# Optimization experiments

Measured on AMD Instinct MI355X. Metric: run time of the kernel, lower is better.

The kernel has to match this reference:

```python
import jax, jax.numpy as jnp
import numpy as np

N = 100000
E = 1600000
F_IN = 602
NHID = 128
N_CLS = 41


def setup_inputs() -> dict:
    key = jax.random.key(0)
    k1, k2, k3, k4 = jax.random.split(key, 4)
    x = jax.random.normal(k1, (N, F_IN), dtype=jnp.float32)
    edge_index = jax.random.randint(k2, (2, E), 0, N, dtype=jnp.int64)
    # Glorot-style scaled weights
    W1 = jax.random.normal(k3, (F_IN, NHID), dtype=jnp.float32) * (1.0 / np.sqrt(F_IN))
    b1 = jnp.zeros((NHID,), dtype=jnp.float32)
    W2 = jax.random.normal(k4, (NHID, N_CLS), dtype=jnp.float32) * (1.0 / np.sqrt(NHID))
    b2 = jnp.zeros((N_CLS,), dtype=jnp.float32)
    return {"x": x, "edge_index": edge_index, "W1": W1, "b1": b1, "W2": W2, "b2": b2}


def reference(x, edge_index, W1, b1, W2, b2):
    n = x.shape[0]
    loop = jnp.arange(n, dtype=edge_index.dtype)
    # PyG GCNConv: add self-loops, symmetric normalization D^-1/2 (A+I) D^-1/2
    src = jnp.concatenate([edge_index[0], loop])  # [E+N]
    dst = jnp.concatenate([edge_index[1], loop])  # [E+N]
    ones = jnp.ones(src.shape[0], dtype=x.dtype)
    deg = jax.ops.segment_sum(ones, dst, num_segments=n)  # in-degree incl self-loop
    dinv = jnp.where(deg > 0, jax.lax.rsqrt(deg), 0.0)
    norm = dinv[src] * dinv[dst]  # [E+N]

    def conv(h, W, b):
        h = h @ W  # transform first (smaller feature dim for gather)
        msg = h[src] * norm[:, None]  # gather + scale
        return jax.ops.segment_sum(msg, dst, num_segments=n) + b  # scatter-add

    h = jax.nn.relu(conv(x, W1, b1))
    # dropout is identity in eval mode
    out = conv(h, W2, b2)
    return jax.nn.log_softmax(out, axis=1)
```

## Files before the change

kernel.cpp:

```cpp
#include <hip/hip_runtime.h>
#include <math.h>

#define GK 602
#define GH 128
#define GC 41
#define GCP 48
#define KPAD 608
#define NKT 19

typedef __bf16 bf16x8 __attribute__((ext_vector_type(8)));
typedef float f32x16 __attribute__((ext_vector_type(16)));

__device__ __forceinline__ unsigned short f2bf(float f) {
    __bf16 b = (__bf16)f;
    return __builtin_bit_cast(unsigned short, b);
}
__device__ __forceinline__ float bf2f(unsigned short u) {
    return __uint_as_float((unsigned int)u << 16);
}
__device__ __forceinline__ float bflo(unsigned int u) { return __uint_as_float(u << 16); }
__device__ __forceinline__ float bfhi(unsigned int u) { return __uint_as_float(u & 0xffff0000u); }

__device__ __forceinline__ void gl_lds16(const float* g, float* l) {
    __builtin_amdgcn_global_load_lds((const __attribute__((address_space(1))) void*)g,
                                     (__attribute__((address_space(3))) void*)l, 16, 0, 0);
}
__device__ __forceinline__ void gl_lds4(const float* g, float* l) {
    __builtin_amdgcn_global_load_lds((const __attribute__((address_space(1))) void*)g,
                                     (__attribute__((address_space(3))) void*)l, 4, 0, 0);
}


__global__ void k_hist(const int* __restrict__ dst, int* __restrict__ counts, int E) {
    int e = blockIdx.x * 256 + threadIdx.x;
    if (e < E) atomicAdd(&counts[dst[e]], 1);
}

__global__ void k_scan_a(const int* __restrict__ counts, int* __restrict__ row_ptr,
                         int* __restrict__ bsum, int n) {
    __shared__ int wsum[4];
    int t = threadIdx.x;
    int lane = t & 63;
    int wv = t >> 6;
    int base = blockIdx.x * 1024 + t * 4;
    int v[4];
    int s = 0;
#pragma unroll
    for (int j = 0; j < 4; ++j) {
        int idx = base + j;
        v[j] = (idx < n) ? counts[idx] : 0;
        s += v[j];
    }
    int incl = s;
#pragma unroll
    for (int o = 1; o < 64; o <<= 1) {
        int x = __shfl_up(incl, o);
        if (lane >= o) incl += x;
    }
    if (lane == 63) wsum[wv] = incl;
    __syncthreads();
    int woff = 0;
#pragma unroll
    for (int i = 0; i < 3; ++i) woff += (i < wv) ? wsum[i] : 0;
    if (t == 255) bsum[blockIdx.x] = woff + incl;
    int off = woff + incl - s;
#pragma unroll
    for (int j = 0; j < 4; ++j) {
        int idx = base + j;
        if (idx < n) row_ptr[idx] = off;
        off += v[j];
    }
}

__global__ void k_scan_b(int* __restrict__ bsum, int nb) {
    __shared__ int sh[256];
    int t = threadIdx.x;
    int v = (t < nb) ? bsum[t] : 0;
    sh[t] = v;
    __syncthreads();
    for (int o = 1; o < 256; o <<= 1) {
        int x = (t >= o) ? sh[t - o] : 0;
        __syncthreads();
        sh[t] += x;
        __syncthreads();
    }
    if (t < nb) bsum[t] = sh[t] - v;
}

__global__ void k_scan_c(int* __restrict__ row_ptr, const int* __restrict__ bsum,
                         const int* __restrict__ counts, float* __restrict__ dinv,
                         int* __restrict__ cursor, int n, int E) {
    int i = blockIdx.x * 256 + threadIdx.x;
    if (i < n) {
        int rp = row_ptr[i] + bsum[i >> 10];
        row_ptr[i] = rp;
        cursor[i] = rp;
        dinv[i] = rsqrtf((float)(counts[i] + 1));
    }
    if (i == 0) row_ptr[n] = E;
}

__global__ void k_fill(const int* __restrict__ src, const int* __restrict__ dst,
                       const float* __restrict__ dinv,
                       int* __restrict__ cursor, int2* __restrict__ meta, int E) {
    int e = blockIdx.x * 256 + threadIdx.x;
    if (e < E) {
        int s = src[e];
        int d = dst[e];
        int p = atomicAdd(&cursor[d], 1);
        float w = dinv[s] * dinv[d];
        meta[p] = make_int2(s, __float_as_int(w));
    }
}


__global__ void k_prepW1F(const float* __restrict__ W1, unsigned short* __restrict__ W1F) {
    int i = blockIdx.x * 256 + threadIdx.x;
    if (i >= NKT * 4096) return;
    int kt = i >> 12;
    int r  = i & 4095;
    int nt = r >> 10;
    int r2 = r & 1023;
    int bs = r2 >> 9;
    int r3 = r2 & 511;
    int ln = r3 >> 3;
    int j  = r3 & 7;
    int col = 32 * nt + (ln & 31);
    int k   = 32 * kt + 16 * bs + 8 * (ln >> 5) + j;
    float v = (k < GK) ? W1[(size_t)k * GH + col] : 0.f;
    W1F[i] = f2bf(v);
}


#define SLABF (32 * GK)
#define CH16  (SLABF / 4)

__global__ __launch_bounds__(256, 2) void k_gemm1_mfma(const float* __restrict__ X,
                                                       const unsigned short* __restrict__ W1F,
                                                       unsigned short* __restrict__ Y, int M) {
    __shared__ float As[SLABF + 16];
    int tid = threadIdx.x;
    int lane = tid & 63;
    int w = tid >> 6;
    int rowBase = blockIdx.x * 32;
    const float* slab = X + (size_t)rowBase * GK;

#pragma unroll
    for (int r = 0; r < 18; ++r) {
        int c = tid + 256 * r;
        gl_lds16(slab + 4 * c, &As[4 * c]);
    }
    if (w < 3) {
        int c = 4608 + (w << 6) + lane;
        gl_lds16(slab + 4 * c, &As[4 * c]);
    } else {
        int f = 19200 + lane;
        gl_lds4(slab + f, &As[f]);
    }
    if (tid < 16) As[SLABF + tid] = 0.f;
    asm volatile("s_waitcnt vmcnt(0)" ::: "memory");
    __syncthreads();

    int arow = lane & 31;
    int kh = 8 * (lane >> 5);
    const float* Ar = &As[arow * GK];
    const unsigned short* Wb = W1F + (size_t)w * 1024 + (size_t)lane * 8;

    f32x16 acc;
#pragma unroll
    for (int i = 0; i < 16; ++i) acc[i] = 0.f;

#pragma unroll
    for (int t = 0; t < NKT; ++t) {
        const unsigned short* Wt = Wb + (size_t)t * 4096;
        bf16x8 b0 = *(const bf16x8*)(Wt);
        bf16x8 b1 = *(const bf16x8*)(Wt + 512);
        const float* a0p = Ar + 32 * t + kh;
        float2 p0 = *(const float2*)(a0p + 0);
        float2 p1 = *(const float2*)(a0p + 2);
        float2 p2 = *(const float2*)(a0p + 4);
        float2 p3 = *(const float2*)(a0p + 6);
        const float* a1p = a0p + 16;
        float2 q0 = *(const float2*)(a1p + 0);
        float2 q1 = *(const float2*)(a1p + 2);
        float2 q2 = *(const float2*)(a1p + 4);
        float2 q3 = *(const float2*)(a1p + 6);
        bf16x8 af0, af1;
        af0[0] = (__bf16)p0.x; af0[1] = (__bf16)p0.y;
        af0[2] = (__bf16)p1.x; af0[3] = (__bf16)p1.y;
        af0[4] = (__bf16)p2.x; af0[5] = (__bf16)p2.y;
        af0[6] = (__bf16)p3.x; af0[7] = (__bf16)p3.y;
        af1[0] = (__bf16)q0.x; af1[1] = (__bf16)q0.y;
        af1[2] = (__bf16)q1.x; af1[3] = (__bf16)q1.y;
        af1[4] = (__bf16)q2.x; af1[5] = (__bf16)q2.y;
        af1[6] = (__bf16)q3.x; af1[7] = (__bf16)q3.y;
        acc = __builtin_amdgcn_mfma_f32_32x32x16_bf16(af0, b0, acc, 0, 0, 0);
        acc = __builtin_amdgcn_mfma_f32_32x32x16_bf16(af1, b1, acc, 0, 0, 0);
    }

    int gcol = 32 * w + (lane & 31);
#pragma unroll
    for (int reg = 0; reg < 16; ++reg) {
        int rrow = (reg & 3) + 8 * (reg >> 2) + 4 * (lane >> 5);
        int grow = rowBase + rrow;
        if (grow < M) Y[(size_t)grow * GH + gcol] = f2bf(acc[reg]);
    }
}


__global__ __launch_bounds__(256) void k_agg1(const unsigned int* __restrict__ H,
                                              unsigned int* __restrict__ O,
                                              const int* __restrict__ row_ptr,
                                              const int2* __restrict__ meta,
                                              const float* __restrict__ dinv,
                                              const float* __restrict__ bias, int n) {
    int wv = threadIdx.x >> 6;
    int lane = threadIdx.x & 63;
    int d = blockIdx.x * 4 + wv;
    if (d >= n) return;
    float dd = dinv[d];
    int beg = row_ptr[d], end = row_ptr[d + 1];
    unsigned int v = H[(size_t)d * 64 + lane];
    float sw = dd * dd;
    float a0 = sw * bflo(v);
    float a1 = sw * bfhi(v);
    int e = beg;
    for (; e + 16 <= end; e += 16) {
        int2 m[16];
        unsigned int u[16];
#pragma unroll
        for (int j = 0; j < 16; ++j) m[j] = meta[e + j];
#pragma unroll
        for (int j = 0; j < 16; ++j) u[j] = H[(size_t)m[j].x * 64 + lane];
#pragma unroll
        for (int j = 0; j < 16; ++j) {
            float wj = __int_as_float(m[j].y);
            a0 = fmaf(wj, bflo(u[j]), a0);
            a1 = fmaf(wj, bfhi(u[j]), a1);
        }
    }
    if (e + 8 <= end) {
        int2 m[8];
        unsigned int u[8];
#pragma unroll
        for (int j = 0; j < 8; ++j) m[j] = meta[e + j];
#pragma unroll
        for (int j = 0; j < 8; ++j) u[j] = H[(size_t)m[j].x * 64 + lane];
#pragma unroll
        for (int j = 0; j < 8; ++j) {
            float wj = __int_as_float(m[j].y);
            a0 = fmaf(wj, bflo(u[j]), a0);
            a1 = fmaf(wj, bfhi(u[j]), a1);
        }
        e += 8;
    }
    if (e + 4 <= end) {
        int2 m[4];
        unsigned int u[4];
#pragma unroll
        for (int j = 0; j < 4; ++j) m[j] = meta[e + j];
#pragma unroll
        for (int j = 0; j < 4; ++j) u[j] = H[(size_t)m[j].x * 64 + lane];
#pragma unroll
        for (int j = 0; j < 4; ++j) {
            float wj = __int_as_float(m[j].y);
            a0 = fmaf(wj, bflo(u[j]), a0);
            a1 = fmaf(wj, bfhi(u[j]), a1);
        }
        e += 4;
    }
    for (; e < end; ++e) {
        int2 m = meta[e];
        unsigned int u = H[(size_t)m.x * 64 + lane];
        float wj = __int_as_float(m.y);
        a0 = fmaf(wj, bflo(u), a0);
        a1 = fmaf(wj, bfhi(u), a1);
    }
    a0 = fmaxf(a0 + bias[2 * lane], 0.f);
    a1 = fmaxf(a1 + bias[2 * lane + 1], 0.f);
    O[(size_t)d * 64 + lane] = (unsigned int)f2bf(a0) | ((unsigned int)f2bf(a1) << 16);
}


__global__ __launch_bounds__(256) void k_gemm2t(const unsigned int* __restrict__ Hb,
                                                const float* __restrict__ W2,
                                                unsigned short* __restrict__ G, int n) {
    __shared__ float ws[128][GCP];
    for (int i = threadIdx.x; i < 128 * GCP; i += 256) {
        int k = i / GCP;
        int c = i - k * GCP;
        ws[k][c] = (c < GC) ? W2[k * GC + c] : 0.f;
    }
    __syncthreads();
    int r0 = blockIdx.x * 512 + threadIdx.x;
    int r1 = r0 + 256;
    bool v0 = r0 < n, v1 = r1 < n;
    float acc0[GCP], acc1[GCP];
#pragma unroll
    for (int c = 0; c < GCP; ++c) { acc0[c] = 0.f; acc1[c] = 0.f; }
    const uint2* h0 = (const uint2*)(Hb + (size_t)(v0 ? r0 : 0) * 64);
    const uint2* h1 = (const uint2*)(Hb + (size_t)(v1 ? r1 : 0) * 64);
    for (int q = 0; q < 32; ++q) {
        uint2 ua = h0[q];
        uint2 ub = h1[q];
        float va[4] = {bflo(ua.x), bfhi(ua.x), bflo(ua.y), bfhi(ua.y)};
        float vb[4] = {bflo(ub.x), bfhi(ub.x), bflo(ub.y), bfhi(ub.y)};
#pragma unroll
        for (int j = 0; j < 4; ++j) {
            int k = 4 * q + j;
#pragma unroll
            for (int cq = 0; cq < GCP / 4; ++cq) {
                float4 wv = *(const float4*)&ws[k][4 * cq];
                acc0[4 * cq + 0] = fmaf(va[j], wv.x, acc0[4 * cq + 0]);
                acc0[4 * cq + 1] = fmaf(va[j], wv.y, acc0[4 * cq + 1]);
                acc0[4 * cq + 2] = fmaf(va[j], wv.z, acc0[4 * cq + 2]);
                acc0[4 * cq + 3] = fmaf(va[j], wv.w, acc0[4 * cq + 3]);
                acc1[4 * cq + 0] = fmaf(vb[j], wv.x, acc1[4 * cq + 0]);
                acc1[4 * cq + 1] = fmaf(vb[j], wv.y, acc1[4 * cq + 1]);
                acc1[4 * cq + 2] = fmaf(vb[j], wv.z, acc1[4 * cq + 2]);
                acc1[4 * cq + 3] = fmaf(vb[j], wv.w, acc1[4 * cq + 3]);
            }
        }
    }
    if (v0) {
#pragma unroll
        for (int c = 0; c < GCP; ++c) G[(size_t)r0 * GCP + c] = f2bf(acc0[c]);
    }
    if (v1) {
#pragma unroll
        for (int c = 0; c < GCP; ++c) G[(size_t)r1 * GCP + c] = f2bf(acc1[c]);
    }
}


__global__ __launch_bounds__(256) void k_agg2(const unsigned short* __restrict__ G,
                                              float* __restrict__ out,
                                              const int* __restrict__ row_ptr,
                                              const int2* __restrict__ meta,
                                              const float* __restrict__ dinv,
                                              const float* __restrict__ b2, int n) {
    int wv = threadIdx.x >> 6;
    int lane = threadIdx.x & 63;
    int gl = (lane < GCP) ? lane : (GCP - 1);
    int d = blockIdx.x * 4 + wv;
    if (d >= n) return;
    float dd = dinv[d];
    int beg = row_ptr[d], end = row_ptr[d + 1];
    float a = dd * dd * bf2f(G[(size_t)d * GCP + gl]);
    int e = beg;
    for (; e + 16 <= end; e += 16) {
        int2 m[16];
        unsigned short u[16];
#pragma unroll
        for (int j = 0; j < 16; ++j) m[j] = meta[e + j];
#pragma unroll
        for (int j = 0; j < 16; ++j) u[j] = G[(size_t)m[j].x * GCP + gl];
#pragma unroll
        for (int j = 0; j < 16; ++j) a = fmaf(__int_as_float(m[j].y), bf2f(u[j]), a);
    }
    if (e + 8 <= end) {
        int2 m[8];
        unsigned short u[8];
#pragma unroll
        for (int j = 0; j < 8; ++j) m[j] = meta[e + j];
#pragma unroll
        for (int j = 0; j < 8; ++j) u[j] = G[(size_t)m[j].x * GCP + gl];
#pragma unroll
        for (int j = 0; j < 8; ++j) a = fmaf(__int_as_float(m[j].y), bf2f(u[j]), a);
        e += 8;
    }
    if (e + 4 <= end) {
        int2 m[4];
        unsigned short u[4];
#pragma unroll
        for (int j = 0; j < 4; ++j) m[j] = meta[e + j];
#pragma unroll
        for (int j = 0; j < 4; ++j) u[j] = G[(size_t)m[j].x * GCP + gl];
#pragma unroll
        for (int j = 0; j < 4; ++j) a = fmaf(__int_as_float(m[j].y), bf2f(u[j]), a);
        e += 4;
    }
    for (; e < end; ++e) {
        int2 m = meta[e];
        a = fmaf(__int_as_float(m.y), bf2f(G[(size_t)m.x * GCP + gl]), a);
    }
    float logit = (lane < GC) ? (a + b2[lane]) : -INFINITY;
    float mx = logit;
#pragma unroll
    for (int off = 32; off; off >>= 1) mx = fmaxf(mx, __shfl_xor(mx, off));
    float ex = (lane < GC) ? __expf(logit - mx) : 0.f;
    float sm = ex;
#pragma unroll
    for (int off = 32; off; off >>= 1) sm += __shfl_xor(sm, off);
    if (lane < GC) out[(size_t)d * GC + lane] = logit - mx - __logf(sm);
}


static inline size_t alignup256(size_t x) { return (x + 255) & ~(size_t)255; }

extern "C" void kernel_launch(void* const* d_in, const int* in_sizes, int n_in,
                              void* d_out, int out_size, void* d_ws, size_t ws_size,
                              hipStream_t stream) {
    const float* x  = (const float*)d_in[0];
    const int*   ei = (const int*)d_in[1];
    const float* W1 = (const float*)d_in[2];
    const float* b1 = (const float*)d_in[3];
    const float* W2 = (const float*)d_in[4];
    const float* b2 = (const float*)d_in[5];
    float* out = (float*)d_out;

    const int n = in_sizes[0] / GK;
    const int E = in_sizes[1] / 2;
    const int* src = ei;
    const int* dst = ei + E;

    char* w = (char*)d_ws;
    char* p;
    p = w; w += alignup256((size_t)n * 4);            float* dinv  = (float*)p;
    p = w; w += alignup256((size_t)n * 4);            int* counts  = (int*)p;
    p = w; w += alignup256((size_t)n * 4);            int* cursor  = (int*)p;
    p = w; w += alignup256((size_t)(n + 1) * 4);      int* row_ptr = (int*)p;
    p = w; w += alignup256(1024 * 4);                 int* bsum    = (int*)p;
    p = w; w += alignup256((size_t)E * 8);            int2* meta   = (int2*)p;
    p = w; w += alignup256((size_t)GH * KPAD * 2);    unsigned short* W1F = (unsigned short*)p;
    p = w; w += alignup256((size_t)n * GH * 2);       unsigned short* bufA = (unsigned short*)p;
    p = w; w += alignup256((size_t)n * GH * 2);       unsigned short* bufB = (unsigned short*)p;
    p = w; w += alignup256((size_t)n * GCP * 2);      unsigned short* G    = (unsigned short*)p;

    hipMemsetAsync(counts, 0, (size_t)n * 4, stream);

    int gE = (E + 255) / 256;
    int gN = (n + 255) / 256;
    int nb = (n + 1023) / 1024;

    k_hist<<<gE, 256, 0, stream>>>(dst, counts, E);
    k_scan_a<<<nb, 256, 0, stream>>>(counts, row_ptr, bsum, n);
    k_scan_b<<<1, 256, 0, stream>>>(bsum, nb);
    k_scan_c<<<gN, 256, 0, stream>>>(row_ptr, bsum, counts, dinv, cursor, n, E);
    k_fill<<<gE, 256, 0, stream>>>(src, dst, dinv, cursor, meta, E);

    k_prepW1F<<<(NKT * 4096 + 255) / 256, 256, 0, stream>>>(W1, W1F);
    k_gemm1_mfma<<<(n + 31) / 32, 256, 0, stream>>>(x, W1F, bufA, n);
    k_agg1<<<(n + 3) / 4, 256, 0, stream>>>((const unsigned int*)bufA, (unsigned int*)bufB,
                                            row_ptr, meta, dinv, b1, n);
    k_gemm2t<<<(n + 511) / 512, 256, 0, stream>>>((const unsigned int*)bufB, W2, G, n);
    k_agg2<<<(n + 3) / 4, 256, 0, stream>>>(G, out, row_ptr, meta, dinv, b2, n);
}
```

Baseline: 679.9 us.

## Fuse second-layer GEMM into layer-1 aggregation and vectorize edge preprocessing

The relu'd layer-1 aggregate for each node is staged in LDS, and a 128x48 matvec against a pre-transposed W2 runs inside the aggregation kernel. This removes the separate gemm2 kernel and the round trip of the hidden bf16 buffer through global memory. The histogram and CSR fill kernels now process four edges per thread using int4 loads. W2 transposition is folded into the weight-prep kernel. The trade-off is extra per-wave work in the aggregation tail, with only 48 of 64 lanes active, and W2T being re-read from global/L2 by every wave.

```diff
diff --git a/kernel.cpp b/kernel.cpp
--- a/kernel.cpp
+++ b/kernel.cpp
@@ -7,6 +7,8 @@
 #define GCP 48
 #define KPAD 608
 #define NKT 19
+#define W1FN (NKT * 4096)
+#define W2TN (GCP * 128)
 
 typedef __bf16 bf16x8 __attribute__((ext_vector_type(8)));
 typedef float f32x16 __attribute__((ext_vector_type(16)));
@@ -32,8 +34,21 @@
 
 
 __global__ void k_hist(const int* __restrict__ dst, int* __restrict__ counts, int E) {
-    int e = blockIdx.x * 256 + threadIdx.x;
-    if (e < E) atomicAdd(&counts[dst[e]], 1);
+    int g = blockIdx.x * 256 + threadIdx.x;
+    int base = g * 4;
+    if (((E & 3) == 0) && (base + 3 < E)) {
+        int4 d4 = *(const int4*)(dst + base);
+        atomicAdd(&counts[d4.x], 1);
+        atomicAdd(&counts[d4.y], 1);
+        atomicAdd(&counts[d4.z], 1);
+        atomicAdd(&counts[d4.w], 1);
+    } else {
+#pragma unroll
+        for (int j = 0; j < 4; ++j) {
+            int e = base + j;
+            if (e < E) atomicAdd(&counts[dst[e]], 1);
+        }
+    }
 }
 
 __global__ void k_scan_a(const int* __restrict__ counts, int* __restrict__ row_ptr,
@@ -103,37 +118,61 @@
 __global__ void k_fill(const int* __restrict__ src, const int* __restrict__ dst,
                        const float* __restrict__ dinv,
                        int* __restrict__ cursor, int2* __restrict__ meta, int E) {
-    int e = blockIdx.x * 256 + threadIdx.x;
-    if (e < E) {
-        int s = src[e];
-        int d = dst[e];
-        int p = atomicAdd(&cursor[d], 1);
-        float w = dinv[s] * dinv[d];
-        meta[p] = make_int2(s, __float_as_int(w));
-    }
-}
-
-
-__global__ void k_prepW1F(const float* __restrict__ W1, unsigned short* __restrict__ W1F) {
+    int g = blockIdx.x * 256 + threadIdx.x;
+    int base = g * 4;
+    if (((E & 3) == 0) && (base + 3 < E)) {
+        int4 s4 = *(const int4*)(src + base);
+        int4 d4 = *(const int4*)(dst + base);
+        int ss[4] = {s4.x, s4.y, s4.z, s4.w};
+        int dd[4] = {d4.x, d4.y, d4.z, d4.w};
+#pragma unroll
+        for (int j = 0; j < 4; ++j) {
+            int p = atomicAdd(&cursor[dd[j]], 1);
+            float w = dinv[ss[j]] * dinv[dd[j]];
+            meta[p] = make_int2(ss[j], __float_as_int(w));
+        }
+    } else {
+#pragma unroll
+        for (int j = 0; j < 4; ++j) {
+            int e = base + j;
+            if (e < E) {
+                int s = src[e];
+                int d = dst[e];
+                int p = atomicAdd(&cursor[d], 1);
+                float w = dinv[s] * dinv[d];
+                meta[p] = make_int2(s, __float_as_int(w));
+            }
+        }
+    }
+}
+
+
+__global__ void k_prepW(const float* __restrict__ W1, unsigned short* __restrict__ W1F,
+                        const float* __restrict__ W2, float* __restrict__ W2T) {
     int i = blockIdx.x * 256 + threadIdx.x;
-    if (i >= NKT * 4096) return;
-    int kt = i >> 12;
-    int r  = i & 4095;
-    int nt = r >> 10;
-    int r2 = r & 1023;
-    int bs = r2 >> 9;
-    int r3 = r2 & 511;
-    int ln = r3 >> 3;
-    int j  = r3 & 7;
-    int col = 32 * nt + (ln & 31);
-    int k   = 32 * kt + 16 * bs + 8 * (ln >> 5) + j;
-    float v = (k < GK) ? W1[(size_t)k * GH + col] : 0.f;
-    W1F[i] = f2bf(v);
+    if (i < W1FN) {
+        int kt = i >> 12;
+        int r  = i & 4095;
+        int nt = r >> 10;
+        int r2 = r & 1023;
+        int bs = r2 >> 9;
+        int r3 = r2 & 511;
+        int ln = r3 >> 3;
+        int j  = r3 & 7;
+        int col = 32 * nt + (ln & 31);
+        int k   = 32 * kt + 16 * bs + 8 * (ln >> 5) + j;
+        float v = (k < GK) ? W1[(size_t)k * GH + col] : 0.f;
+        W1F[i] = f2bf(v);
+    } else if (i < W1FN + W2TN) {
+        int j = i - W1FN;
+        int c = j >> 7;
+        int k = j & 127;
+        W2T[j] = (c < GC) ? W2[k * GC + c] : 0.f;
+    }
 }
 
 
 #define SLABF (32 * GK)
-#define CH16  (SLABF / 4)
 
 __global__ __launch_bounds__(256, 2) void k_gemm1_mfma(const float* __restrict__ X,
                                                        const unsigned short* __restrict__ W1F,
@@ -208,12 +247,14 @@
 }
 
 
-__global__ __launch_bounds__(256) void k_agg1(const unsigned int* __restrict__ H,
-                                              unsigned int* __restrict__ O,
-                                              const int* __restrict__ row_ptr,
-                                              const int2* __restrict__ meta,
-                                              const float* __restrict__ dinv,
-                                              const float* __restrict__ bias, int n) {
+__global__ __launch_bounds__(256) void k_agg1f(const unsigned int* __restrict__ H,
+                                               unsigned short* __restrict__ G,
+                                               const int* __restrict__ row_ptr,
+                                               const int2* __restrict__ meta,
+                                               const float* __restrict__ dinv,
+                                               const float* __restrict__ bias,
+                                               const float* __restrict__ W2T, int n) {
+    __shared__ float hs[4][128];
     int wv = threadIdx.x >> 6;
     int lane = threadIdx.x & 63;
     int d = blockIdx.x * 4 + wv;
@@ -278,57 +319,26 @@
     }
     a0 = fmaxf(a0 + bias[2 * lane], 0.f);
     a1 = fmaxf(a1 + bias[2 * lane + 1], 0.f);
-    O[(size_t)d * 64 + lane] = (unsigned int)f2bf(a0) | ((unsigned int)f2bf(a1) << 16);
-}
-
-
-__global__ __launch_bounds__(256) void k_gemm2t(const unsigned int* __restrict__ Hb,
-                                                const float* __restrict__ W2,
-                                                unsigned short* __restrict__ G, int n) {
-    __shared__ float ws[128][GCP];
-    for (int i = threadIdx.x; i < 128 * GCP; i += 256) {
-        int k = i / GCP;
-        int c = i - k * GCP;
-        ws[k][c] = (c < GC) ? W2[k * GC + c] : 0.f;
-    }
-    __syncthreads();
-    int r0 = blockIdx.x * 512 + threadIdx.x;
-    int r1 = r0 + 256;
-    bool v0 = r0 < n, v1 = r1 < n;
-    float acc0[GCP], acc1[GCP];
-#pragma unroll
-    for (int c = 0; c < GCP; ++c) { acc0[c] = 0.f; acc1[c] = 0.f; }
-    const uint2* h0 = (const uint2*)(Hb + (size_t)(v0 ? r0 : 0) * 64);
-    const uint2* h1 = (const uint2*)(Hb + (size_t)(v1 ? r1 : 0) * 64);
-    for (int q = 0; q < 32; ++q) {
-        uint2 ua = h0[q];
-        uint2 ub = h1[q];
-        float va[4] = {bflo(ua.x), bfhi(ua.x), bflo(ua.y), bfhi(ua.y)};
-        float vb[4] = {bflo(ub.x), bfhi(ub.x), bflo(ub.y), bfhi(ub.y)};
-#pragma unroll
-        for (int j = 0; j < 4; ++j) {
-            int k = 4 * q + j;
-#pragma unroll
-            for (int cq = 0; cq < GCP / 4; ++cq) {
-                float4 wv = *(const float4*)&ws[k][4 * cq];
-                acc0[4 * cq + 0] = fmaf(va[j], wv.x, acc0[4 * cq + 0]);
-                acc0[4 * cq + 1] = fmaf(va[j], wv.y, acc0[4 * cq + 1]);
-                acc0[4 * cq + 2] = fmaf(va[j], wv.z, acc0[4 * cq + 2]);
-                acc0[4 * cq + 3] = fmaf(va[j], wv.w, acc0[4 * cq + 3]);
-                acc1[4 * cq + 0] = fmaf(vb[j], wv.x, acc1[4 * cq + 0]);
-                acc1[4 * cq + 1] = fmaf(vb[j], wv.y, acc1[4 * cq + 1]);
-                acc1[4 * cq + 2] = fmaf(vb[j], wv.z, acc1[4 * cq + 2]);
-                acc1[4 * cq + 3] = fmaf(vb[j], wv.w, acc1[4 * cq + 3]);
-            }
-        }
-    }
-    if (v0) {
-#pragma unroll
-        for (int c = 0; c < GCP; ++c) G[(size_t)r0 * GCP + c] = f2bf(acc0[c]);
-    }
-    if (v1) {
-#pragma unroll
-        for (int c = 0; c < GCP; ++c) G[(size_t)r1 * GCP + c] = f2bf(acc1[c]);
+
+    *(float2*)&hs[wv][2 * lane] = make_float2(a0, a1);
+    asm volatile("s_waitcnt lgkmcnt(0)" ::: "memory");
+    __builtin_amdgcn_sched_barrier(0);
+
+    if (lane < GCP) {
+        const float* wr = W2T + (size_t)lane * 128;
+        float s0 = 0.f, s1 = 0.f;
+#pragma unroll
+        for (int q = 0; q < 16; ++q) {
+            float4 wv0 = *(const float4*)(wr + 8 * q);
+            float4 wv1 = *(const float4*)(wr + 8 * q + 4);
+            float4 h0 = *(const float4*)&hs[wv][8 * q];
+            float4 h1 = *(const float4*)&hs[wv][8 * q + 4];
+            s0 = fmaf(wv0.x, h0.x, s0); s0 = fmaf(wv0.y, h0.y, s0);
+            s0 = fmaf(wv0.z, h0.z, s0); s0 = fmaf(wv0.w, h0.w, s0);
+            s1 = fmaf(wv1.x, h1.x, s1); s1 = fmaf(wv1.y, h1.y, s1);
+            s1 = fmaf(wv1.z, h1.z, s1); s1 = fmaf(wv1.w, h1.w, s1);
+        }
+        G[(size_t)d * GCP + lane] = f2bf(s0 + s1);
     }
 }
 
@@ -423,26 +433,25 @@
     p = w; w += alignup256(1024 * 4);                 int* bsum    = (int*)p;
     p = w; w += alignup256((size_t)E * 8);            int2* meta   = (int2*)p;
     p = w; w += alignup256((size_t)GH * KPAD * 2);    unsigned short* W1F = (unsigned short*)p;
+    p = w; w += alignup256((size_t)W2TN * 4);         float* W2T = (float*)p;
     p = w; w += alignup256((size_t)n * GH * 2);       unsigned short* bufA = (unsigned short*)p;
-    p = w; w += alignup256((size_t)n * GH * 2);       unsigned short* bufB = (unsigned short*)p;
     p = w; w += alignup256((size_t)n * GCP * 2);      unsigned short* G    = (unsigned short*)p;
 
     hipMemsetAsync(counts, 0, (size_t)n * 4, stream);
 
-    int gE = (E + 255) / 256;
+    int gE4 = (E + 1023) / 1024;
     int gN = (n + 255) / 256;
     int nb = (n + 1023) / 1024;
 
-    k_hist<<<gE, 256, 0, stream>>>(dst, counts, E);
+    k_hist<<<gE4, 256, 0, stream>>>(dst, counts, E);
     k_scan_a<<<nb, 256, 0, stream>>>(counts, row_ptr, bsum, n);
     k_scan_b<<<1, 256, 0, stream>>>(bsum, nb);
     k_scan_c<<<gN, 256, 0, stream>>>(row_ptr, bsum, counts, dinv, cursor, n, E);
-    k_fill<<<gE, 256, 0, stream>>>(src, dst, dinv, cursor, meta, E);
-
-    k_prepW1F<<<(NKT * 4096 + 255) / 256, 256, 0, stream>>>(W1, W1F);
+    k_fill<<<gE4, 256, 0, stream>>>(src, dst, dinv, cursor, meta, E);
+
+    k_prepW<<<(W1FN + W2TN + 255) / 256, 256, 0, stream>>>(W1, W1F, W2, W2T);
     k_gemm1_mfma<<<(n + 31) / 32, 256, 0, stream>>>(x, W1F, bufA, n);
-    k_agg1<<<(n + 3) / 4, 256, 0, stream>>>((const unsigned int*)bufA, (unsigned int*)bufB,
-                                            row_ptr, meta, dinv, b1, n);
-    k_gemm2t<<<(n + 511) / 512, 256, 0, stream>>>((const unsigned int*)bufB, W2, G, n);
+    k_agg1f<<<(n + 3) / 4, 256, 0, stream>>>((const unsigned int*)bufA, G,
+                                             row_ptr, meta, dinv, b1, W2T, n);
     k_agg2<<<(n + 3) / 4, 256, 0, stream>>>(G, out, row_ptr, meta, dinv, b2, n);
 }
```

After: 906.8 us. +33.4%, slower.

## Store only source indices in CSR and recompute edge weights from dinv in aggregation

Applied to the files above, without the earlier changes.

The CSR edge array now stores only the source index (4 bytes) instead of an (index, weight) pair (8 bytes). The aggregation kernels gather dinv[src] per edge and apply the destination's dinv once at the end, rather than reading a precomputed per-edge weight. The hist and fill kernels also process four edges per thread with int4 loads, and fill no longer reads dinv. This halves edge-metadata traffic and the fill's scattered writes, at the cost of an extra random 4-byte gather per edge in both aggregation passes.

```diff
diff --git a/kernel.cpp b/kernel.cpp
--- a/kernel.cpp
+++ b/kernel.cpp
@@ -32,8 +32,21 @@
 
 
 __global__ void k_hist(const int* __restrict__ dst, int* __restrict__ counts, int E) {
-    int e = blockIdx.x * 256 + threadIdx.x;
-    if (e < E) atomicAdd(&counts[dst[e]], 1);
+    int g = blockIdx.x * 256 + threadIdx.x;
+    int base = g * 4;
+    if (((E & 3) == 0) && (base + 3 < E)) {
+        int4 d4 = *(const int4*)(dst + base);
+        atomicAdd(&counts[d4.x], 1);
+        atomicAdd(&counts[d4.y], 1);
+        atomicAdd(&counts[d4.z], 1);
+        atomicAdd(&counts[d4.w], 1);
+    } else {
+#pragma unroll
+        for (int j = 0; j < 4; ++j) {
+            int e = base + j;
+            if (e < E) atomicAdd(&counts[dst[e]], 1);
+        }
+    }
 }
 
 __global__ void k_scan_a(const int* __restrict__ counts, int* __restrict__ row_ptr,
@@ -101,15 +114,28 @@
 }
 
 __global__ void k_fill(const int* __restrict__ src, const int* __restrict__ dst,
-                       const float* __restrict__ dinv,
-                       int* __restrict__ cursor, int2* __restrict__ meta, int E) {
-    int e = blockIdx.x * 256 + threadIdx.x;
-    if (e < E) {
-        int s = src[e];
-        int d = dst[e];
-        int p = atomicAdd(&cursor[d], 1);
-        float w = dinv[s] * dinv[d];
-        meta[p] = make_int2(s, __float_as_int(w));
+                       int* __restrict__ cursor, int* __restrict__ meta, int E) {
+    int g = blockIdx.x * 256 + threadIdx.x;
+    int base = g * 4;
+    if (((E & 3) == 0) && (base + 3 < E)) {
+        int4 s4 = *(const int4*)(src + base);
+        int4 d4 = *(const int4*)(dst + base);
+        int ss[4] = {s4.x, s4.y, s4.z, s4.w};
+        int dd[4] = {d4.x, d4.y, d4.z, d4.w};
+#pragma unroll
+        for (int j = 0; j < 4; ++j) {
+            int p = atomicAdd(&cursor[dd[j]], 1);
+            meta[p] = ss[j];
+        }
+    } else {
+#pragma unroll
+        for (int j = 0; j < 4; ++j) {
+            int e = base + j;
+            if (e < E) {
+                int p = atomicAdd(&cursor[dst[e]], 1);
+                meta[p] = src[e];
+            }
+        }
     }
 }
 
@@ -133,7 +159,6 @@
 
 
 #define SLABF (32 * GK)
-#define CH16  (SLABF / 4)
 
 __global__ __launch_bounds__(256, 2) void k_gemm1_mfma(const float* __restrict__ X,
                                                        const unsigned short* __restrict__ W1F,
@@ -211,7 +236,7 @@
 __global__ __launch_bounds__(256) void k_agg1(const unsigned int* __restrict__ H,
                                               unsigned int* __restrict__ O,
                                               const int* __restrict__ row_ptr,
-                                              const int2* __restrict__ meta,
+                                              const int* __restrict__ meta,
                                               const float* __restrict__ dinv,
                                               const float* __restrict__ bias, int n) {
     int wv = threadIdx.x >> 6;
@@ -221,63 +246,68 @@
     float dd = dinv[d];
     int beg = row_ptr[d], end = row_ptr[d + 1];
     unsigned int v = H[(size_t)d * 64 + lane];
-    float sw = dd * dd;
-    float a0 = sw * bflo(v);
-    float a1 = sw * bfhi(v);
+    float a0 = dd * bflo(v);
+    float a1 = dd * bfhi(v);
     int e = beg;
     for (; e + 16 <= end; e += 16) {
-        int2 m[16];
+        int m[16];
         unsigned int u[16];
+        float ws[16];
 #pragma unroll
         for (int j = 0; j < 16; ++j) m[j] = meta[e + j];
 #pragma unroll
-        for (int j = 0; j < 16; ++j) u[j] = H[(size_t)m[j].x * 64 + lane];
+        for (int j = 0; j < 16; ++j) u[j] = H[(size_t)m[j] * 64 + lane];
+#pragma unroll
+        for (int j = 0; j < 16; ++j) ws[j] = dinv[m[j]];
 #pragma unroll
         for (int j = 0; j < 16; ++j) {
-            float wj = __int_as_float(m[j].y);
-            a0 = fmaf(wj, bflo(u[j]), a0);
-            a1 = fmaf(wj, bfhi(u[j]), a1);
+            a0 = fmaf(ws[j], bflo(u[j]), a0);
+            a1 = fmaf(ws[j], bfhi(u[j]), a1);
         }
     }
     if (e + 8 <= end) {
-        int2 m[8];
+        int m[8];
         unsigned int u[8];
+        float ws[8];
 #pragma unroll
         for (int j = 0; j < 8; ++j) m[j] = meta[e + j];
 #pragma unroll
-        for (int j = 0; j < 8; ++j) u[j] = H[(size_t)m[j].x * 64 + lane];
+        for (int j = 0; j < 8; ++j) u[j] = H[(size_t)m[j] * 64 + lane];
+#pragma unroll
+        for (int j = 0; j < 8; ++j) ws[j] = dinv[m[j]];
 #pragma unroll
         for (int j = 0; j < 8; ++j) {
-            float wj = __int_as_float(m[j].y);
-            a0 = fmaf(wj, bflo(u[j]), a0);
-            a1 = fmaf(wj, bfhi(u[j]), a1);
+            a0 = fmaf(ws[j], bflo(u[j]), a0);
+            a1 = fmaf(ws[j], bfhi(u[j]), a1);
         }
         e += 8;
     }
     if (e + 4 <= end) {
-        int2 m[4];
+        int m[4];
         unsigned int u[4];
+        float ws[4];
 #pragma unroll
         for (int j = 0; j < 4; ++j) m[j] = meta[e + j];
 #pragma unroll
-        for (int j = 0; j < 4; ++j) u[j] = H[(size_t)m[j].x * 64 + lane];
+        for (int j = 0; j < 4; ++j) u[j] = H[(size_t)m[j] * 64 + lane];
+#pragma unroll
+        for (int j = 0; j < 4; ++j) ws[j] = dinv[m[j]];
 #pragma unroll
         for (int j = 0; j < 4; ++j) {
-            float wj = __int_as_float(m[j].y);
-            a0 = fmaf(wj, bflo(u[j]), a0);
-            a1 = fmaf(wj, bfhi(u[j]), a1);
+            a0 = fmaf(ws[j], bflo(u[j]), a0);
+            a1 = fmaf(ws[j], bfhi(u[j]), a1);
         }
         e += 4;
     }
     for (; e < end; ++e) {
-        int2 m = meta[e];
-        unsigned int u = H[(size_t)m.x * 64 + lane];
-        float wj = __int_as_float(m.y);
+        int m = meta[e];
+        unsigned int u = H[(size_t)m * 64 + lane];
+        float wj = dinv[m];
         a0 = fmaf(wj, bflo(u), a0);
         a1 = fmaf(wj, bfhi(u), a1);
     }
-    a0 = fmaxf(a0 + bias[2 * lane], 0.f);
-    a1 = fmaxf(a1 + bias[2 * lane + 1], 0.f);
+    a0 = fmaxf(fmaf(dd, a0, bias[2 * lane]), 0.f);
+    a1 = fmaxf(fmaf(dd, a1, bias[2 * lane + 1]), 0.f);
     O[(size_t)d * 64 + lane] = (unsigned int)f2bf(a0) | ((unsigned int)f2bf(a1) << 16);
 }
 
@@ -336,7 +366,7 @@
 __global__ __launch_bounds__(256) void k_agg2(const unsigned short* __restrict__ G,
                                               float* __restrict__ out,
                                               const int* __restrict__ row_ptr,
-                                              const int2* __restrict__ meta,
+                                              const int* __restrict__ meta,
                                               const float* __restrict__ dinv,
                                               const float* __restrict__ b2, int n) {
     int wv = threadIdx.x >> 6;
@@ -346,45 +376,54 @@
     if (d >= n) return;
     float dd = dinv[d];
     int beg = row_ptr[d], end = row_ptr[d + 1];
-    float a = dd * dd * bf2f(G[(size_t)d * GCP + gl]);
+    float a = dd * bf2f(G[(size_t)d * GCP + gl]);
     int e = beg;
     for (; e + 16 <= end; e += 16) {
-        int2 m[16];
+        int m[16];
         unsigned short u[16];
+        float ws[16];
 #pragma unroll
         for (int j = 0; j < 16; ++j) m[j] = meta[e + j];
 #pragma unroll
-        for (int j = 0; j < 16; ++j) u[j] = G[(size_t)m[j].x * GCP + gl];
-#pragma unroll
-        for (int j = 0; j < 16; ++j) a = fmaf(__int_as_float(m[j].y), bf2f(u[j]), a);
+        for (int j = 0; j < 16; ++j) u[j] = G[(size_t)m[j] * GCP + gl];
+#pragma unroll
+        for (int j = 0; j < 16; ++j) ws[j] = dinv[m[j]];
+#pragma unroll
+        for (int j = 0; j < 16; ++j) a = fmaf(ws[j], bf2f(u[j]), a);
     }
     if (e + 8 <= end) {
-        int2 m[8];
+        int m[8];
         unsigned short u[8];
+        float ws[8];
 #pragma unroll
         for (int j = 0; j < 8; ++j) m[j] = meta[e + j];
 #pragma unroll
-        for (int j = 0; j < 8; ++j) u[j] = G[(size_t)m[j].x * GCP + gl];
-#pragma unroll
-        for (int j = 0; j < 8; ++j) a = fmaf(__int_as_float(m[j].y), bf2f(u[j]), a);
+        for (int j = 0; j < 8; ++j) u[j] = G[(size_t)m[j] * GCP + gl];
+#pragma unroll
+        for (int j = 0; j < 8; ++j) ws[j] = dinv[m[j]];
+#pragma unroll
+        for (int j = 0; j < 8; ++j) a = fmaf(ws[j], bf2f(u[j]), a);
         e += 8;
     }
     if (e + 4 <= end) {
-        int2 m[4];
+        int m[4];
         unsigned short u[4];
+        float ws[4];
 #pragma unroll
         for (int j = 0; j < 4; ++j) m[j] = meta[e + j];
 #pragma unroll
-        for (int j = 0; j < 4; ++j) u[j] = G[(size_t)m[j].x * GCP + gl];
-#pragma unroll
-        for (int j = 0; j < 4; ++j) a = fmaf(__int_as_float(m[j].y), bf2f(u[j]), a);
+        for (int j = 0; j < 4; ++j) u[j] = G[(size_t)m[j] * GCP + gl];
+#pragma unroll
+        for (int j = 0; j < 4; ++j) ws[j] = dinv[m[j]];
+#pragma unroll
+        for (int j = 0; j < 4; ++j) a = fmaf(ws[j], bf2f(u[j]), a);
         e += 4;
     }
     for (; e < end; ++e) {
-        int2 m = meta[e];
-        a = fmaf(__int_as_float(m.y), bf2f(G[(size_t)m.x * GCP + gl]), a);
-    }
-    float logit = (lane < GC) ? (a + b2[lane]) : -INFINITY;
+        int m = meta[e];
+        a = fmaf(dinv[m], bf2f(G[(size_t)m * GCP + gl]), a);
+    }
+    float logit = (lane < GC) ? fmaf(dd, a, b2[lane]) : -INFINITY;
     float mx = logit;
 #pragma unroll
     for (int off = 32; off; off >>= 1) mx = fmaxf(mx, __shfl_xor(mx, off));
@@ -421,7 +460,7 @@
     p = w; w += alignup256((size_t)n * 4);            int* cursor  = (int*)p;
     p = w; w += alignup256((size_t)(n + 1) * 4);      int* row_ptr = (int*)p;
     p = w; w += alignup256(1024 * 4);                 int* bsum    = (int*)p;
-    p = w; w += alignup256((size_t)E * 8);            int2* meta   = (int2*)p;
+    p = w; w += alignup256((size_t)E * 4);            int* meta    = (int*)p;
     p = w; w += alignup256((size_t)GH * KPAD * 2);    unsigned short* W1F = (unsigned short*)p;
     p = w; w += alignup256((size_t)n * GH * 2);       unsigned short* bufA = (unsigned short*)p;
     p = w; w += alignup256((size_t)n * GH * 2);       unsigned short* bufB = (unsigned short*)p;
@@ -429,15 +468,15 @@
 
     hipMemsetAsync(counts, 0, (size_t)n * 4, stream);
 
-    int gE = (E + 255) / 256;
+    int gE4 = (E + 1023) / 1024;
     int gN = (n + 255) / 256;
     int nb = (n + 1023) / 1024;
 
-    k_hist<<<gE, 256, 0, stream>>>(dst, counts, E);
+    k_hist<<<gE4, 256, 0, stream>>>(dst, counts, E);
     k_scan_a<<<nb, 256, 0, stream>>>(counts, row_ptr, bsum, n);
     k_scan_b<<<1, 256, 0, stream>>>(bsum, nb);
     k_scan_c<<<gN, 256, 0, stream>>>(row_ptr, bsum, counts, dinv, cursor, n, E);
-    k_fill<<<gE, 256, 0, stream>>>(src, dst, dinv, cursor, meta, E);
+    k_fill<<<gE4, 256, 0, stream>>>(src, dst, cursor, meta, E);
 
     k_prepW1F<<<(NKT * 4096 + 255) / 256, 256, 0, stream>>>(W1, W1F);
     k_gemm1_mfma<<<(n + 31) / 32, 256, 0, stream>>>(x, W1F, bufA, n);
```

Measured after the change: 763.9 us. +12.3%, slower.

## Merge W1 prep with histogram and CSR fill with GEMM1 via block-range dispatch

Applied to the files above, without the earlier changes.

Fuses the W1 bf16 reformat and the degree histogram into one launch, and fuses the CSR fill pass into the GEMM1 launch, using disjoint block ranges so the independent work can run concurrently. Each histogram/fill thread now handles four edges with vectorized int4 loads. This removes two kernel launches and lets the latency-bound atomic scatter overlap with the compute-heavy GEMM. The fill blocks inherit GEMM1's launch bounds and its shared-memory allocation, which may reduce their occupancy.

```diff
diff --git a/kernel.cpp b/kernel.cpp
--- a/kernel.cpp
+++ b/kernel.cpp
@@ -7,6 +7,7 @@
 #define GCP 48
 #define KPAD 608
 #define NKT 19
+#define W1FN (NKT * 4096)
 
 typedef __bf16 bf16x8 __attribute__((ext_vector_type(8)));
 typedef float f32x16 __attribute__((ext_vector_type(16)));
@@ -31,9 +32,41 @@
 }
 
 
-__global__ void k_hist(const int* __restrict__ dst, int* __restrict__ counts, int E) {
-    int e = blockIdx.x * 256 + threadIdx.x;
-    if (e < E) atomicAdd(&counts[dst[e]], 1);
+__global__ void k_pre(const float* __restrict__ W1, unsigned short* __restrict__ W1F,
+                      const int* __restrict__ dst, int* __restrict__ counts,
+                      int E, int nbPrep) {
+    if ((int)blockIdx.x < nbPrep) {
+        int i = blockIdx.x * 256 + threadIdx.x;
+        if (i >= W1FN) return;
+        int kt = i >> 12;
+        int r  = i & 4095;
+        int nt = r >> 10;
+        int r2 = r & 1023;
+        int bs = r2 >> 9;
+        int r3 = r2 & 511;
+        int ln = r3 >> 3;
+        int j  = r3 & 7;
+        int col = 32 * nt + (ln & 31);
+        int k   = 32 * kt + 16 * bs + 8 * (ln >> 5) + j;
+        float v = (k < GK) ? W1[(size_t)k * GH + col] : 0.f;
+        W1F[i] = f2bf(v);
+    } else {
+        int g = (blockIdx.x - nbPrep) * 256 + threadIdx.x;
+        int base = g * 4;
+        if (((E & 3) == 0) && (base + 3 < E)) {
+            int4 d4 = *(const int4*)(dst + base);
+            atomicAdd(&counts[d4.x], 1);
+            atomicAdd(&counts[d4.y], 1);
+            atomicAdd(&counts[d4.z], 1);
+            atomicAdd(&counts[d4.w], 1);
+        } else {
+#pragma unroll
+            for (int j2 = 0; j2 < 4; ++j2) {
+                int e = base + j2;
+                if (e < E) atomicAdd(&counts[dst[e]], 1);
+            }
+        }
+    }
 }
 
 __global__ void k_scan_a(const int* __restrict__ counts, int* __restrict__ row_ptr,
@@ -100,44 +133,45 @@
     if (i == 0) row_ptr[n] = E;
 }
 
-__global__ void k_fill(const int* __restrict__ src, const int* __restrict__ dst,
-                       const float* __restrict__ dinv,
-                       int* __restrict__ cursor, int2* __restrict__ meta, int E) {
-    int e = blockIdx.x * 256 + threadIdx.x;
-    if (e < E) {
-        int s = src[e];
-        int d = dst[e];
-        int p = atomicAdd(&cursor[d], 1);
-        float w = dinv[s] * dinv[d];
-        meta[p] = make_int2(s, __float_as_int(w));
-    }
-}
-
-
-__global__ void k_prepW1F(const float* __restrict__ W1, unsigned short* __restrict__ W1F) {
-    int i = blockIdx.x * 256 + threadIdx.x;
-    if (i >= NKT * 4096) return;
-    int kt = i >> 12;
-    int r  = i & 4095;
-    int nt = r >> 10;
-    int r2 = r & 1023;
-    int bs = r2 >> 9;
-    int r3 = r2 & 511;
-    int ln = r3 >> 3;
-    int j  = r3 & 7;
-    int col = 32 * nt + (ln & 31);
-    int k   = 32 * kt + 16 * bs + 8 * (ln >> 5) + j;
-    float v = (k < GK) ? W1[(size_t)k * GH + col] : 0.f;
-    W1F[i] = f2bf(v);
-}
-
 
 #define SLABF (32 * GK)
-#define CH16  (SLABF / 4)
-
-__global__ __launch_bounds__(256, 2) void k_gemm1_mfma(const float* __restrict__ X,
-                                                       const unsigned short* __restrict__ W1F,
-                                                       unsigned short* __restrict__ Y, int M) {
+
+__global__ __launch_bounds__(256, 2) void k_gemm1_fill(
+        const float* __restrict__ X, const unsigned short* __restrict__ W1F,
+        unsigned short* __restrict__ Y, int M,
+        const int* __restrict__ src, const int* __restrict__ dst,
+        const float* __restrict__ dinv, int* __restrict__ cursor,
+        int2* __restrict__ meta, int E, int nbG) {
+    if ((int)blockIdx.x >= nbG) {
+        int g = (blockIdx.x - nbG) * 256 + threadIdx.x;
+        int base = g * 4;
+        if (((E & 3) == 0) && (base + 3 < E)) {
+            int4 s4 = *(const int4*)(src + base);
+            int4 d4 = *(const int4*)(dst + base);
+            int ss[4] = {s4.x, s4.y, s4.z, s4.w};
+            int dd[4] = {d4.x, d4.y, d4.z, d4.w};
+#pragma unroll
+            for (int j = 0; j < 4; ++j) {
+                int p = atomicAdd(&cursor[dd[j]], 1);
+                float w = dinv[ss[j]] * dinv[dd[j]];
+                meta[p] = make_int2(ss[j], __float_as_int(w));
+            }
+        } else {
+#pragma unroll
+            for (int j = 0; j < 4; ++j) {
+                int e = base + j;
+                if (e < E) {
+                    int s = src[e];
+                    int d = dst[e];
+                    int p = atomicAdd(&cursor[d], 1);
+                    float w = dinv[s] * dinv[d];
+                    meta[p] = make_int2(s, __float_as_int(w));
+                }
+            }
+        }
+        return;
+    }
+
     __shared__ float As[SLABF + 16];
     int tid = threadIdx.x;
     int lane = tid & 63;
@@ -429,18 +463,19 @@
 
     hipMemsetAsync(counts, 0, (size_t)n * 4, stream);
 
-    int gE = (E + 255) / 256;
     int gN = (n + 255) / 256;
     int nb = (n + 1023) / 1024;
-
-    k_hist<<<gE, 256, 0, stream>>>(dst, counts, E);
+    int nbPrep = (W1FN + 255) / 256;
+    int nbHist = (E / 4 + 255) / 256;
+    int nbG    = (n + 31) / 32;
+
+    k_pre<<<nbPrep + nbHist, 256, 0, stream>>>(W1, W1F, dst, counts, E, nbPrep);
     k_scan_a<<<nb, 256, 0, stream>>>(counts, row_ptr, bsum, n);
     k_scan_b<<<1, 256, 0, stream>>>(bsum, nb);
     k_scan_c<<<gN, 256, 0, stream>>>(row_ptr, bsum, counts, dinv, cursor, n, E);
-    k_fill<<<gE, 256, 0, stream>>>(src, dst, dinv, cursor, meta, E);
-
-    k_prepW1F<<<(NKT * 4096 + 255) / 256, 256, 0, stream>>>(W1, W1F);
-    k_gemm1_mfma<<<(n + 31) / 32, 256, 0, stream>>>(x, W1F, bufA, n);
+
+    k_gemm1_fill<<<nbG + nbHist, 256, 0, stream>>>(x, W1F, bufA, n,
+                                                   src, dst, dinv, cursor, meta, E, nbG);
     k_agg1<<<(n + 3) / 4, 256, 0, stream>>>((const unsigned int*)bufA, (unsigned int*)bufB,
                                             row_ptr, meta, dinv, b1, n);
     k_gemm2t<<<(n + 511) / 512, 256, 0, stream>>>((const unsigned int*)bufB, W2, G, n);
```

New measurement: 668.5 us. About the same (-1.7%).
